# Kernel tuning notes

Hardware: AMD Instinct MI355X
Metric: run time of the kernel (lower is better)

## Reference

```python
import jax, jax.numpy as jnp
import numpy as np


def _grid_sample_bilinear(tex, grid):
    """Faithful torch.nn.functional.grid_sample(mode='bilinear', padding_mode='zeros', align_corners=False).
    tex:  [C, Hin, Win] (single texture, broadcast over grid batch)
    grid: [B, Ho, Wo, 2] with (..., 0)=x, (..., 1)=y in [-1, 1]
    returns [B, C, Ho, Wo]
    """
    C, Hin, Win = tex.shape
    # align_corners=False: pixel = ((g + 1) * size - 1) / 2
    gx = ((grid[..., 0] + 1.0) * Win - 1.0) * 0.5
    gy = ((grid[..., 1] + 1.0) * Hin - 1.0) * 0.5
    x0 = jnp.floor(gx)
    y0 = jnp.floor(gy)
    x1 = x0 + 1.0
    y1 = y0 + 1.0
    wx1 = gx - x0
    wx0 = 1.0 - wx1
    wy1 = gy - y0
    wy0 = 1.0 - wy1
    t = jnp.moveaxis(tex, 0, -1)

    def corner(xi, yi, w):
        valid = (xi >= 0) & (xi < Win) & (yi >= 0) & (yi < Hin)  # zero padding
        xc = jnp.clip(xi, 0, Win - 1).astype(jnp.int32)
        yc = jnp.clip(yi, 0, Hin - 1).astype(jnp.int32)
        v = t[yc, xc]  # [B, Ho, Wo, C]
        return v * (w * valid)[..., None]

    out = (corner(x0, y0, wx0 * wy0) + corner(x1, y0, wx1 * wy0)
           + corner(x0, y1, wx0 * wy1) + corner(x1, y1, wx1 * wy1))
    return jnp.moveaxis(out, -1, 1)  # [B, C, Ho, Wo]


def setup_inputs() -> dict:
    key = jax.random.key(0)
    ks = jax.random.split(key, 6)
    TEX_SIZE, C, NR_TEX = 1024, 8, 4
    B, H, W = 1, 2048, 2048
    uv_tensor = jax.random.uniform(ks[0], (B, 2, H, W), dtype=jnp.float32)
    texs = {}
    for i in range(NR_TEX):
        s = TEX_SIZE // (2 ** i)
        texs[f"tex{i}"] = jax.random.normal(ks[1 + i], (C, s, s), dtype=jnp.float32) * 0.1
    return {"uv_tensor": uv_tensor, "iter_nr": 0, **texs}


def reference(uv_tensor, iter_nr, tex0, tex1, tex2, tex3):
    # uv_tensor: [B, 2, H, W] -> channels-last grid in [-1, 1]
    grid = jnp.transpose(uv_tensor, (0, 2, 3, 1)) * 2.0 - 1.0  # [B, H, W, 2]
    x = 0.0
    for tex in (tex0, tex1, tex2, tex3):  # multi-resolution pyramid sum
        x = x + _grid_sample_bilinear(tex, grid)
    return x.astype(jnp.float32)
```

## Files before the change

### kernel.cpp

```cpp
#include <hip/hip_runtime.h>

static constexpr int HOUT = 2048, WOUT = 2048;
static constexpr int NPIX = HOUT * WOUT;

static constexpr size_t N0 = 1024 * 1024, N1 = 512 * 512, N2 = 256 * 256, N3 = 128 * 128;

template <int S, int LOG2S>
__global__ __launch_bounds__(256) void build_pairs(const float* __restrict__ in,
                                                   float* __restrict__ out) {
    int idx = blockIdx.x * 256 + threadIdx.x;
    if (idx >= S * S) return;
    int x = idx & (S - 1);
    int y = idx >> LOG2S;
    const int n = S * S;
    bool v = (x + 1) < S;
    int xc = v ? (x + 1) : (S - 1);
    float l[8], r[8];
#pragma unroll
    for (int c = 0; c < 8; ++c) l[c] = in[c * n + idx];
#pragma unroll
    for (int c = 0; c < 8; ++c) {
        float t = in[c * n + y * S + xc];
        r[c] = v ? t : 0.0f;
    }
    float4* o = reinterpret_cast<float4*>(out + (size_t)idx * 16);
    o[0] = make_float4(l[0], l[1], l[2], l[3]);
    o[1] = make_float4(l[4], l[5], l[6], l[7]);
    o[2] = make_float4(r[0], r[1], r[2], r[3]);
    o[3] = make_float4(r[4], r[5], r[6], r[7]);
}

__global__ __launch_bounds__(256) void transpose_tex(const float* __restrict__ in,
                                                     float* __restrict__ out,
                                                     int n ) {
    int idx = blockIdx.x * blockDim.x + threadIdx.x;
    if (idx >= n) return;
    float4 a, b;
    a.x = in[0 * n + idx];
    a.y = in[1 * n + idx];
    a.z = in[2 * n + idx];
    a.w = in[3 * n + idx];
    b.x = in[4 * n + idx];
    b.y = in[5 * n + idx];
    b.z = in[6 * n + idx];
    b.w = in[7 * n + idx];
    float4* o = reinterpret_cast<float4*>(out + (size_t)idx * 8);
    o[0] = a;
    o[1] = b;
}

__device__ __forceinline__ void fma4(float4& acc, const float4 v, const float w) {
    acc.x = fmaf(v.x, w, acc.x);
    acc.y = fmaf(v.y, w, acc.y);
    acc.z = fmaf(v.z, w, acc.z);
    acc.w = fmaf(v.w, w, acc.w);
}

template <int S>
__device__ __forceinline__ void sample_level_pair(const float* __restrict__ p,
                                                  float u, float v,
                                                  float4& acc0, float4& acc1) {
    float gxn = u * 2.0f - 1.0f;
    float gyn = v * 2.0f - 1.0f;
    float gx = ((gxn + 1.0f) * (float)S - 1.0f) * 0.5f;
    float gy = ((gyn + 1.0f) * (float)S - 1.0f) * 0.5f;
    float x0f = floorf(gx);
    float y0f = floorf(gy);
    float wx1 = gx - x0f, wx0 = 1.0f - wx1;
    float wy1 = gy - y0f, wy0 = 1.0f - wy1;
    int x0 = (int)x0f, y0 = (int)y0f;
    int x1 = x0 + 1, y1 = y0 + 1;

    int qx = min(max(x0, 0), S - 1);
    int ry0 = min(max(y0, 0), S - 1);
    int ry1 = min(max(y1, 0), S - 1);

    float ws0, ws1;
    if (x0 < 0) {
        ws0 = wx1;
        ws1 = 0.0f;
    } else if (x0 >= S) {
        ws0 = 0.0f;
        ws1 = 0.0f;
    } else {
        ws0 = wx0;
        ws1 = (x1 < S) ? wx1 : 0.0f;
    }
    float wt = (y0 >= 0 && y0 < S) ? wy0 : 0.0f;
    float wb = (y1 < S) ? wy1 : 0.0f;

    const float4* pt = reinterpret_cast<const float4*>(p + ((size_t)ry0 * S + qx) * 16);
    const float4* pb = reinterpret_cast<const float4*>(p + ((size_t)ry1 * S + qx) * 16);
    float4 tl0 = pt[0], tl1 = pt[1], tr0 = pt[2], tr1 = pt[3];
    float4 bl0 = pb[0], bl1 = pb[1], br0 = pb[2], br1 = pb[3];

    float wtl = ws0 * wt, wtr = ws1 * wt;
    float wbl = ws0 * wb, wbr = ws1 * wb;

    fma4(acc0, tl0, wtl); fma4(acc1, tl1, wtl);
    fma4(acc0, tr0, wtr); fma4(acc1, tr1, wtr);
    fma4(acc0, bl0, wbl); fma4(acc1, bl1, wbl);
    fma4(acc0, br0, wbr); fma4(acc1, br1, wbr);
}

template <int S>
__device__ __forceinline__ void sample_level_cl(const float* __restrict__ t,
                                                float u, float v,
                                                float4& acc0, float4& acc1) {
    float gxn = u * 2.0f - 1.0f;
    float gyn = v * 2.0f - 1.0f;
    float gx = ((gxn + 1.0f) * (float)S - 1.0f) * 0.5f;
    float gy = ((gyn + 1.0f) * (float)S - 1.0f) * 0.5f;
    float x0f = floorf(gx);
    float y0f = floorf(gy);
    float wx1 = gx - x0f, wx0 = 1.0f - wx1;
    float wy1 = gy - y0f, wy0 = 1.0f - wy1;
    int x0 = (int)x0f, y0 = (int)y0f;
    int x1 = x0 + 1, y1 = y0 + 1;

    bool vx0 = (x0 >= 0) && (x0 < S);
    bool vx1 = (x1 >= 0) && (x1 < S);
    bool vy0 = (y0 >= 0) && (y0 < S);
    bool vy1 = (y1 >= 0) && (y1 < S);

    int cx0 = min(max(x0, 0), S - 1);
    int cx1 = min(max(x1, 0), S - 1);
    int cy0 = min(max(y0, 0), S - 1);
    int cy1 = min(max(y1, 0), S - 1);

    float w00 = (vx0 && vy0) ? wx0 * wy0 : 0.0f;
    float w10 = (vx1 && vy0) ? wx1 * wy0 : 0.0f;
    float w01 = (vx0 && vy1) ? wx0 * wy1 : 0.0f;
    float w11 = (vx1 && vy1) ? wx1 * wy1 : 0.0f;

    const float4* p00 = reinterpret_cast<const float4*>(t + ((size_t)cy0 * S + cx0) * 8);
    const float4* p10 = reinterpret_cast<const float4*>(t + ((size_t)cy0 * S + cx1) * 8);
    const float4* p01 = reinterpret_cast<const float4*>(t + ((size_t)cy1 * S + cx0) * 8);
    const float4* p11 = reinterpret_cast<const float4*>(t + ((size_t)cy1 * S + cx1) * 8);

    float4 t00a = p00[0], t00b = p00[1];
    float4 t10a = p10[0], t10b = p10[1];
    float4 t01a = p01[0], t01b = p01[1];
    float4 t11a = p11[0], t11b = p11[1];

    fma4(acc0, t00a, w00); fma4(acc1, t00b, w00);
    fma4(acc0, t10a, w10); fma4(acc1, t10b, w10);
    fma4(acc0, t01a, w01); fma4(acc1, t01b, w01);
    fma4(acc0, t11a, w11); fma4(acc1, t11b, w11);
}

__global__ __launch_bounds__(256) void deferred_main_pair(const float* __restrict__ uv,
                                                          const float* __restrict__ p0,
                                                          const float* __restrict__ p1,
                                                          const float* __restrict__ t2,
                                                          const float* __restrict__ t3,
                                                          float* __restrict__ out) {
    int pix = blockIdx.x * blockDim.x + threadIdx.x;
    if (pix >= NPIX) return;
    float u = uv[pix];
    float v = uv[NPIX + pix];

    float4 acc0 = {0.f, 0.f, 0.f, 0.f};
    float4 acc1 = {0.f, 0.f, 0.f, 0.f};

    sample_level_pair<1024>(p0, u, v, acc0, acc1);
    sample_level_pair<512>(p1, u, v, acc0, acc1);
    sample_level_cl<256>(t2, u, v, acc0, acc1);
    sample_level_cl<128>(t3, u, v, acc0, acc1);

    out[0 * NPIX + pix] = acc0.x;
    out[1 * NPIX + pix] = acc0.y;
    out[2 * NPIX + pix] = acc0.z;
    out[3 * NPIX + pix] = acc0.w;
    out[4 * NPIX + pix] = acc1.x;
    out[5 * NPIX + pix] = acc1.y;
    out[6 * NPIX + pix] = acc1.z;
    out[7 * NPIX + pix] = acc1.w;
}

__global__ __launch_bounds__(256) void deferred_main_cl(const float* __restrict__ uv,
                                                        const float* __restrict__ t0,
                                                        const float* __restrict__ t1,
                                                        const float* __restrict__ t2,
                                                        const float* __restrict__ t3,
                                                        float* __restrict__ out) {
    int pix = blockIdx.x * blockDim.x + threadIdx.x;
    if (pix >= NPIX) return;
    float u = uv[pix];
    float v = uv[NPIX + pix];
    float4 acc0 = {0.f, 0.f, 0.f, 0.f};
    float4 acc1 = {0.f, 0.f, 0.f, 0.f};
    sample_level_cl<1024>(t0, u, v, acc0, acc1);
    sample_level_cl<512>(t1, u, v, acc0, acc1);
    sample_level_cl<256>(t2, u, v, acc0, acc1);
    sample_level_cl<128>(t3, u, v, acc0, acc1);
    out[0 * NPIX + pix] = acc0.x;
    out[1 * NPIX + pix] = acc0.y;
    out[2 * NPIX + pix] = acc0.z;
    out[3 * NPIX + pix] = acc0.w;
    out[4 * NPIX + pix] = acc1.x;
    out[5 * NPIX + pix] = acc1.y;
    out[6 * NPIX + pix] = acc1.z;
    out[7 * NPIX + pix] = acc1.w;
}

template <int S>
__device__ __forceinline__ void sample_level_chw(const float* __restrict__ t,
                                                 float u, float v,
                                                 float* __restrict__ acc) {
    float gxn = u * 2.0f - 1.0f;
    float gyn = v * 2.0f - 1.0f;
    float gx = ((gxn + 1.0f) * (float)S - 1.0f) * 0.5f;
    float gy = ((gyn + 1.0f) * (float)S - 1.0f) * 0.5f;
    float x0f = floorf(gx);
    float y0f = floorf(gy);
    float wx1 = gx - x0f, wx0 = 1.0f - wx1;
    float wy1 = gy - y0f, wy0 = 1.0f - wy1;
    int x0 = (int)x0f, y0 = (int)y0f;
    int x1 = x0 + 1, y1 = y0 + 1;
    bool vx0 = (x0 >= 0) && (x0 < S);
    bool vx1 = (x1 >= 0) && (x1 < S);
    bool vy0 = (y0 >= 0) && (y0 < S);
    bool vy1 = (y1 >= 0) && (y1 < S);
    int cx0 = min(max(x0, 0), S - 1);
    int cx1 = min(max(x1, 0), S - 1);
    int cy0 = min(max(y0, 0), S - 1);
    int cy1 = min(max(y1, 0), S - 1);
    float w00 = (vx0 && vy0) ? wx0 * wy0 : 0.0f;
    float w10 = (vx1 && vy0) ? wx1 * wy0 : 0.0f;
    float w01 = (vx0 && vy1) ? wx0 * wy1 : 0.0f;
    float w11 = (vx1 && vy1) ? wx1 * wy1 : 0.0f;
    size_t o00 = (size_t)cy0 * S + cx0;
    size_t o10 = (size_t)cy0 * S + cx1;
    size_t o01 = (size_t)cy1 * S + cx0;
    size_t o11 = (size_t)cy1 * S + cx1;
#pragma unroll
    for (int c = 0; c < 8; ++c) {
        const float* tc = t + (size_t)c * S * S;
        float s = tc[o00] * w00 + tc[o10] * w10 + tc[o01] * w01 + tc[o11] * w11;
        acc[c] += s;
    }
}

__global__ __launch_bounds__(256) void deferred_fallback(const float* __restrict__ uv,
                                                         const float* __restrict__ t0,
                                                         const float* __restrict__ t1,
                                                         const float* __restrict__ t2,
                                                         const float* __restrict__ t3,
                                                         float* __restrict__ out) {
    int pix = blockIdx.x * blockDim.x + threadIdx.x;
    if (pix >= NPIX) return;
    float u = uv[pix];
    float v = uv[NPIX + pix];
    float acc[8] = {0.f, 0.f, 0.f, 0.f, 0.f, 0.f, 0.f, 0.f};
    sample_level_chw<1024>(t0, u, v, acc);
    sample_level_chw<512>(t1, u, v, acc);
    sample_level_chw<256>(t2, u, v, acc);
    sample_level_chw<128>(t3, u, v, acc);
#pragma unroll
    for (int c = 0; c < 8; ++c) out[(size_t)c * NPIX + pix] = acc[c];
}

extern "C" void kernel_launch(void* const* d_in, const int* in_sizes, int n_in,
                              void* d_out, int out_size, void* d_ws, size_t ws_size,
                              hipStream_t stream) {
    const float* uv   = (const float*)d_in[0];
    const float* tex0 = (const float*)d_in[2];
    const float* tex1 = (const float*)d_in[3];
    const float* tex2 = (const float*)d_in[4];
    const float* tex3 = (const float*)d_in[5];
    float* out = (float*)d_out;

    const int blk = 256;
    const size_t need_pair = (N0 + N1) * 16 * sizeof(float) + (N2 + N3) * 8 * sizeof(float);
    const size_t need_cl   = (N0 + N1 + N2 + N3) * 8 * sizeof(float);

    if (ws_size >= need_pair) {
        float* p0 = (float*)d_ws;
        float* p1 = p0 + N0 * 16;
        float* c2 = p1 + N1 * 16;
        float* c3 = c2 + N2 * 8;
        build_pairs<1024, 10><<<(int)(N0 / blk), blk, 0, stream>>>(tex0, p0);
        build_pairs<512, 9><<<(int)(N1 / blk), blk, 0, stream>>>(tex1, p1);
        transpose_tex<<<(int)(N2 / blk), blk, 0, stream>>>(tex2, c2, (int)N2);
        transpose_tex<<<(int)(N3 / blk), blk, 0, stream>>>(tex3, c3, (int)N3);
        deferred_main_pair<<<NPIX / blk, blk, 0, stream>>>(uv, p0, p1, c2, c3, out);
    } else if (ws_size >= need_cl) {
        float* w0 = (float*)d_ws;
        float* w1 = w0 + N0 * 8;
        float* w2 = w1 + N1 * 8;
        float* w3 = w2 + N2 * 8;
        transpose_tex<<<(int)(N0 / blk), blk, 0, stream>>>(tex0, w0, (int)N0);
        transpose_tex<<<(int)(N1 / blk), blk, 0, stream>>>(tex1, w1, (int)N1);
        transpose_tex<<<(int)(N2 / blk), blk, 0, stream>>>(tex2, w2, (int)N2);
        transpose_tex<<<(int)(N3 / blk), blk, 0, stream>>>(tex3, w3, (int)N3);
        deferred_main_cl<<<NPIX / blk, blk, 0, stream>>>(uv, w0, w1, w2, w3, out);
    } else {
        deferred_fallback<<<NPIX / blk, blk, 0, stream>>>(uv, tex0, tex1, tex2, tex3, out);
    }
}
```

Baseline: 667.7 us.

## Store 2x2 texel quads in fp16 for the two largest texture levels

The pair layout for levels 0 and 1 becomes a quad layout: each texel entry now holds all four bilinear corners (8 channels each) packed as fp16, 64 bytes per entry. A sample then needs one contiguous 64-byte read instead of two 64-byte fp32 reads from different rows, which cuts gather traffic. Edge handling is rewritten so row indices clamp to S-2 with weights adjusted. The cost is fp16 precision on texture values, which may break tolerance, and a build kernel that does a second scattered write per texel.

New measurement: 536.0 us. 19.7% less time.

```diff
diff --git a/kernel.cpp b/kernel.cpp
--- a/kernel.cpp
+++ b/kernel.cpp
@@ -1,4 +1,5 @@
 #include <hip/hip_runtime.h>
+#include <hip/hip_fp16.h>
 
 static constexpr int HOUT = 2048, WOUT = 2048;
 static constexpr int NPIX = HOUT * WOUT;
@@ -6,28 +7,41 @@
 static constexpr size_t N0 = 1024 * 1024, N1 = 512 * 512, N2 = 256 * 256, N3 = 128 * 128;
 
 template <int S, int LOG2S>
-__global__ __launch_bounds__(256) void build_pairs(const float* __restrict__ in,
-                                                   float* __restrict__ out) {
+__global__ __launch_bounds__(256) void build_quad_h(const float* __restrict__ in,
+                                                    uint4* __restrict__ out) {
     int idx = blockIdx.x * 256 + threadIdx.x;
     if (idx >= S * S) return;
     int x = idx & (S - 1);
     int y = idx >> LOG2S;
     const int n = S * S;
-    bool v = (x + 1) < S;
-    int xc = v ? (x + 1) : (S - 1);
+    bool hv = (x + 1) < S;
+    int ridx = hv ? (idx + 1) : idx;
     float l[8], r[8];
 #pragma unroll
     for (int c = 0; c < 8; ++c) l[c] = in[c * n + idx];
 #pragma unroll
     for (int c = 0; c < 8; ++c) {
-        float t = in[c * n + y * S + xc];
-        r[c] = v ? t : 0.0f;
-    }
-    float4* o = reinterpret_cast<float4*>(out + (size_t)idx * 16);
-    o[0] = make_float4(l[0], l[1], l[2], l[3]);
-    o[1] = make_float4(l[4], l[5], l[6], l[7]);
-    o[2] = make_float4(r[0], r[1], r[2], r[3]);
-    o[3] = make_float4(r[4], r[5], r[6], r[7]);
+        float t = in[c * n + ridx];
+        r[c] = hv ? t : 0.0f;
+    }
+    uint lu[4], ru[4];
+#pragma unroll
+    for (int k = 0; k < 4; ++k) {
+        lu[k] = (uint)__half_as_ushort(__float2half(l[2 * k])) |
+                ((uint)__half_as_ushort(__float2half(l[2 * k + 1])) << 16);
+        ru[k] = (uint)__half_as_ushort(__float2half(r[2 * k])) |
+                ((uint)__half_as_ushort(__float2half(r[2 * k + 1])) << 16);
+    }
+    uint4 lo = make_uint4(lu[0], lu[1], lu[2], lu[3]);
+    uint4 hi = make_uint4(ru[0], ru[1], ru[2], ru[3]);
+    uint4* base = out + (size_t)idx * 4;
+    base[0] = lo;
+    base[1] = hi;
+    if (y > 0) {
+        uint4* up = out + ((size_t)idx - S) * 4;
+        up[2] = lo;
+        up[3] = hi;
+    }
 }
 
 __global__ __launch_bounds__(256) void transpose_tex(const float* __restrict__ in,
@@ -56,8 +70,24 @@
     acc.w = fmaf(v.w, w, acc.w);
 }
 
+__device__ __forceinline__ void fmah(float4& a0, float4& a1, uint4 t, float w) {
+    float2 f;
+    f = __half22float2(__builtin_bit_cast(__half2, t.x));
+    a0.x = fmaf(f.x, w, a0.x);
+    a0.y = fmaf(f.y, w, a0.y);
+    f = __half22float2(__builtin_bit_cast(__half2, t.y));
+    a0.z = fmaf(f.x, w, a0.z);
+    a0.w = fmaf(f.y, w, a0.w);
+    f = __half22float2(__builtin_bit_cast(__half2, t.z));
+    a1.x = fmaf(f.x, w, a1.x);
+    a1.y = fmaf(f.y, w, a1.y);
+    f = __half22float2(__builtin_bit_cast(__half2, t.w));
+    a1.z = fmaf(f.x, w, a1.z);
+    a1.w = fmaf(f.y, w, a1.w);
+}
+
 template <int S>
-__device__ __forceinline__ void sample_level_pair(const float* __restrict__ p,
+__device__ __forceinline__ void sample_level_quad(const uint4* __restrict__ q,
                                                   float u, float v,
                                                   float4& acc0, float4& acc1) {
     float gxn = u * 2.0f - 1.0f;
@@ -69,38 +99,45 @@
     float wx1 = gx - x0f, wx0 = 1.0f - wx1;
     float wy1 = gy - y0f, wy0 = 1.0f - wy1;
     int x0 = (int)x0f, y0 = (int)y0f;
-    int x1 = x0 + 1, y1 = y0 + 1;
-
-    int qx = min(max(x0, 0), S - 1);
-    int ry0 = min(max(y0, 0), S - 1);
-    int ry1 = min(max(y1, 0), S - 1);
-
-    float ws0, ws1;
+
+    int qx;
+    float wc0, wc1;
     if (x0 < 0) {
-        ws0 = wx1;
-        ws1 = 0.0f;
-    } else if (x0 >= S) {
-        ws0 = 0.0f;
-        ws1 = 0.0f;
+        qx = 0;
+        wc0 = wx1;
+        wc1 = 0.0f;
     } else {
-        ws0 = wx0;
-        ws1 = (x1 < S) ? wx1 : 0.0f;
-    }
-    float wt = (y0 >= 0 && y0 < S) ? wy0 : 0.0f;
-    float wb = (y1 < S) ? wy1 : 0.0f;
-
-    const float4* pt = reinterpret_cast<const float4*>(p + ((size_t)ry0 * S + qx) * 16);
-    const float4* pb = reinterpret_cast<const float4*>(p + ((size_t)ry1 * S + qx) * 16);
-    float4 tl0 = pt[0], tl1 = pt[1], tr0 = pt[2], tr1 = pt[3];
-    float4 bl0 = pb[0], bl1 = pb[1], br0 = pb[2], br1 = pb[3];
-
-    float wtl = ws0 * wt, wtr = ws1 * wt;
-    float wbl = ws0 * wb, wbr = ws1 * wb;
-
-    fma4(acc0, tl0, wtl); fma4(acc1, tl1, wtl);
-    fma4(acc0, tr0, wtr); fma4(acc1, tr1, wtr);
-    fma4(acc0, bl0, wbl); fma4(acc1, bl1, wbl);
-    fma4(acc0, br0, wbr); fma4(acc1, br1, wbr);
+        qx = min(x0, S - 1);
+        bool vx = (x0 < S);
+        wc0 = vx ? wx0 : 0.0f;
+        wc1 = vx ? wx1 : 0.0f;
+    }
+    int qy;
+    float wr0, wr1;
+    if (y0 < 0) {
+        qy = 0;
+        wr0 = wy1;
+        wr1 = 0.0f;
+    } else if (y0 >= S - 1) {
+        qy = S - 2;
+        wr0 = 0.0f;
+        wr1 = (y0 == S - 1) ? wy0 : 0.0f;
+    } else {
+        qy = y0;
+        wr0 = wy0;
+        wr1 = wy1;
+    }
+
+    const uint4* e = q + ((size_t)qy * S + qx) * 4;
+    uint4 a = e[0], b = e[1], c = e[2], d = e[3];
+
+    float w00 = wc0 * wr0, w01 = wc1 * wr0;
+    float w10 = wc0 * wr1, w11 = wc1 * wr1;
+
+    fmah(acc0, acc1, a, w00);
+    fmah(acc0, acc1, b, w01);
+    fmah(acc0, acc1, c, w10);
+    fmah(acc0, acc1, d, w11);
 }
 
 template <int S>
@@ -149,9 +186,9 @@
     fma4(acc0, t11a, w11); fma4(acc1, t11b, w11);
 }
 
-__global__ __launch_bounds__(256) void deferred_main_pair(const float* __restrict__ uv,
-                                                          const float* __restrict__ p0,
-                                                          const float* __restrict__ p1,
+__global__ __launch_bounds__(256) void deferred_main_quad(const float* __restrict__ uv,
+                                                          const uint4* __restrict__ q0,
+                                                          const uint4* __restrict__ q1,
                                                           const float* __restrict__ t2,
                                                           const float* __restrict__ t3,
                                                           float* __restrict__ out) {
@@ -163,8 +200,8 @@
     float4 acc0 = {0.f, 0.f, 0.f, 0.f};
     float4 acc1 = {0.f, 0.f, 0.f, 0.f};
 
-    sample_level_pair<1024>(p0, u, v, acc0, acc1);
-    sample_level_pair<512>(p1, u, v, acc0, acc1);
+    sample_level_quad<1024>(q0, u, v, acc0, acc1);
+    sample_level_quad<512>(q1, u, v, acc0, acc1);
     sample_level_cl<256>(t2, u, v, acc0, acc1);
     sample_level_cl<128>(t3, u, v, acc0, acc1);
 
@@ -272,19 +309,19 @@
     float* out = (float*)d_out;
 
     const int blk = 256;
-    const size_t need_pair = (N0 + N1) * 16 * sizeof(float) + (N2 + N3) * 8 * sizeof(float);
+    const size_t need_quad = (N0 + N1) * 64 + (N2 + N3) * 8 * sizeof(float);
     const size_t need_cl   = (N0 + N1 + N2 + N3) * 8 * sizeof(float);
 
-    if (ws_size >= need_pair) {
-        float* p0 = (float*)d_ws;
-        float* p1 = p0 + N0 * 16;
-        float* c2 = p1 + N1 * 16;
+    if (ws_size >= need_quad) {
+        uint4* q0 = (uint4*)d_ws;
+        uint4* q1 = q0 + N0 * 4;
+        float* c2 = (float*)(q1 + N1 * 4);
         float* c3 = c2 + N2 * 8;
-        build_pairs<1024, 10><<<(int)(N0 / blk), blk, 0, stream>>>(tex0, p0);
-        build_pairs<512, 9><<<(int)(N1 / blk), blk, 0, stream>>>(tex1, p1);
+        build_quad_h<1024, 10><<<(int)(N0 / blk), blk, 0, stream>>>(tex0, q0);
+        build_quad_h<512, 9><<<(int)(N1 / blk), blk, 0, stream>>>(tex1, q1);
         transpose_tex<<<(int)(N2 / blk), blk, 0, stream>>>(tex2, c2, (int)N2);
         transpose_tex<<<(int)(N3 / blk), blk, 0, stream>>>(tex3, c3, (int)N3);
-        deferred_main_pair<<<NPIX / blk, blk, 0, stream>>>(uv, p0, p1, c2, c3, out);
+        deferred_main_quad<<<NPIX / blk, blk, 0, stream>>>(uv, q0, q1, c2, c3, out);
     } else if (ws_size >= need_cl) {
         float* w0 = (float*)d_ws;
         float* w1 = w0 + N0 * 8;
```
